# Performance work log

Measured on AMD Instinct MI355X. Metric: run time of the kernel, lower is better.

## Reference

```python
import jax, jax.numpy as jnp
from jax import lax
import numpy as np

NA, NC = 3, 1
CONF_THRESH, IOU_THRESH = 0.5, 0.5


def _conv(x, w, b, pad):
    y = lax.conv_general_dilated(x, w, (1, 1), [(pad, pad), (pad, pad)],
                                 dimension_numbers=('NCHW', 'OIHW', 'NCHW'))
    return y + b[None, :, None, None]


def _maxpool2(x):
    return lax.reduce_window(x, -jnp.inf, lax.max, (1, 1, 2, 2), (1, 1, 2, 2), 'VALID')


def _stream(x, w1, b1, w2, b2):
    x = _maxpool2(jax.nn.relu(_conv(x, w1, b1, 1)))
    x = _maxpool2(jax.nn.relu(_conv(x, w2, b2, 1)))
    return x


def _pairwise_iou(b):
    # b: [N,4] in (x1,y1,x2,y2); matches torchvision box_iou (no area clamp)
    x1, y1, x2, y2 = b[:, 0], b[:, 1], b[:, 2], b[:, 3]
    area = (x2 - x1) * (y2 - y1)
    ix1 = jnp.maximum(x1[:, None], x1[None, :])
    iy1 = jnp.maximum(y1[:, None], y1[None, :])
    ix2 = jnp.minimum(x2[:, None], x2[None, :])
    iy2 = jnp.minimum(y2[:, None], y2[None, :])
    inter = jnp.clip(ix2 - ix1, 0.0) * jnp.clip(iy2 - iy1, 0.0)
    return inter / (area[:, None] + area[None, :] - inter)


def _nms_keep(boxes, scores, conf_keep, iou_thresh):
    # Greedy NMS over a fixed, small N; returns bool keep mask (conf + NMS).
    n = boxes.shape[0]
    order = jnp.argsort(-jnp.where(conf_keep, scores, -jnp.inf))
    iou = _pairwise_iou(boxes[order])  # [N,N] in score order
    idx = jnp.arange(n)

    def body(i, state):
        keep, suppressed = state
        valid = jnp.logical_not(suppressed[i])
        keep = keep.at[i].set(valid)
        suppressed = suppressed | (valid & (iou[i] > iou_thresh) & (idx > i))
        return keep, suppressed

    keep_sorted, _ = lax.fori_loop(0, n, body,
                                   (jnp.zeros(n, bool), jnp.zeros(n, bool)))
    keep = jnp.zeros(n, bool).at[order].set(keep_sorted)
    return keep & conf_keep


def setup_inputs() -> dict:
    key = jax.random.key(0)
    ks = jax.random.split(key, 14)
    s = 0.05
    inp = {
        'x': jax.random.normal(ks[0], (8, 3, 512, 512), jnp.float32),
        'rgb_w1': jax.random.normal(ks[1], (32, 3, 3, 3), jnp.float32) * s,
        'rgb_b1': jnp.zeros((32,), jnp.float32),
        'rgb_w2': jax.random.normal(ks[2], (64, 32, 3, 3), jnp.float32) * s,
        'rgb_b2': jnp.zeros((64,), jnp.float32),
        'ir_w1': jax.random.normal(ks[3], (32, 3, 3, 3), jnp.float32) * s,
        'ir_b1': jnp.zeros((32,), jnp.float32),
        'ir_w2': jax.random.normal(ks[4], (64, 32, 3, 3), jnp.float32) * s,
        'ir_b2': jnp.zeros((64,), jnp.float32),
        'fuse_w': jax.random.normal(ks[5], (128, 128, 3, 3), jnp.float32) * s,
        'fuse_b': jnp.zeros((128,), jnp.float32),
        'det_w': jax.random.normal(ks[6], (NA * (5 + NC), 128, 1, 1), jnp.float32),
        'det_b': jax.random.normal(ks[7], (NA * (5 + NC),), jnp.float32),
    }
    return inp


def reference(x, rgb_w1, rgb_b1, rgb_w2, rgb_b2,
              ir_w1, ir_b1, ir_w2, ir_b2,
              fuse_w, fuse_b, det_w, det_b):
    f1 = _stream(x, rgb_w1, rgb_b1, rgb_w2, rgb_b2)   # [B,64,H/4,W/4]
    f2 = _stream(x, ir_w1, ir_b1, ir_w2, ir_b2)       # [B,64,H/4,W/4]
    f = jnp.concatenate([f1, f2], axis=1)             # [B,128,H/4,W/4]
    f = jax.nn.relu(_conv(f, fuse_w, fuse_b, 1))
    f = jnp.mean(f, axis=(2, 3), keepdims=True)       # AdaptiveAvgPool2d((1,1))
    p = _conv(f, det_w, det_b, 0)                     # [B,18,1,1]
    B, C, H, W = p.shape
    p = p.reshape(B, NA, 5 + NC, H, W).transpose(0, 1, 3, 4, 2)  # [B,na,H,W,5+nc]
    boxes = p[..., :4].reshape(B, -1, 4)              # [B, na*H*W, 4]
    scores = jax.nn.sigmoid(p[..., 4]).reshape(B, -1) # [B, na*H*W]
    conf_keep = scores > CONF_THRESH
    keep = jax.vmap(_nms_keep, in_axes=(0, 0, 0, None))(boxes, scores, conf_keep,
                                                        IOU_THRESH)
    # Fixed-shape equivalent of the per-image variable-length preds list:
    # preds[b] == boxes[b][keep[b]].
    return p, boxes, scores, keep
```

## Files before the change

kernel.cpp:

```cpp
#include <hip/hip_runtime.h>
#include <math.h>


typedef __bf16 bf16x8 __attribute__((ext_vector_type(8)));
typedef float f32x4 __attribute__((ext_vector_type(4)));

static __device__ __forceinline__ ushort f2bf(float f) {
    unsigned u = __float_as_uint(f);
    unsigned r = (u + 0x7fffu + ((u >> 16) & 1u)) >> 16;
    return (ushort)r;
}
static __device__ __forceinline__ float bf2f(ushort h) {
    return __uint_as_float(((unsigned)h) << 16);
}

__global__ __launch_bounds__(256) void conv1_pool(
    const float* __restrict__ x, const float* __restrict__ w,
    const float* __restrict__ bias, ushort* __restrict__ C1h,
    ushort* __restrict__ C1l)
{
    __shared__ float s[3 * 34 * 34];
    const int b = blockIdx.z;
    const int tileX = blockIdx.x, tileY = blockIdx.y;
    const int tid = threadIdx.x;
    const int tx = tid & 15, ty = tid >> 4;
    const int ih0 = tileY * 32 - 1, iw0 = tileX * 32 - 1;

    for (int i = tid; i < 3 * 34 * 34; i += 256) {
        int c = i / 1156, r = i % 1156;
        int y = r / 34, xx = r % 34;
        int ih = ih0 + y, iw = iw0 + xx;
        float v = 0.f;
        if (ih >= 0 && ih < 512 && iw >= 0 && iw < 512)
            v = x[((b * 3 + c) * 512 + ih) * 512 + iw];
        s[i] = v;
    }
    __syncthreads();

    float in[3][4][4];
#pragma unroll
    for (int c = 0; c < 3; ++c)
#pragma unroll
        for (int dy = 0; dy < 4; ++dy)
#pragma unroll
            for (int dx = 0; dx < 4; ++dx)
                in[c][dy][dx] = s[c * 1156 + (2 * ty + dy) * 34 + (2 * tx + dx)];

    const int oh = tileY * 16 + ty, ow = tileX * 16 + tx;
    __attribute__((aligned(16))) ushort hb[32];
    __attribute__((aligned(16))) ushort lb[32];
#pragma unroll
    for (int oc = 0; oc < 32; ++oc) {
        const float bv = bias[oc];
        float m = -INFINITY;
#pragma unroll
        for (int py = 0; py < 2; ++py)
#pragma unroll
            for (int px = 0; px < 2; ++px) {
                float a = 0.f;
#pragma unroll
                for (int c = 0; c < 3; ++c)
#pragma unroll
                    for (int ky = 0; ky < 3; ++ky)
#pragma unroll
                        for (int kx = 0; kx < 3; ++kx)
                            a = fmaf(w[((oc * 3 + c) * 3 + ky) * 3 + kx],
                                     in[c][py + ky][px + kx], a);
                m = fmaxf(m, a);
            }
        m = fmaxf(m + bv, 0.f);
        ushort h = f2bf(m);
        hb[oc] = h;
        lb[oc] = f2bf(m - bf2f(h));
    }
    size_t base = ((size_t)((b * 256 + oh) * 256 + ow)) << 5;
    uint4* dh = (uint4*)(C1h + base);
    uint4* dl = (uint4*)(C1l + base);
#pragma unroll
    for (int k = 0; k < 4; ++k) {
        dh[k] = *(const uint4*)&hb[k * 8];
        dl[k] = *(const uint4*)&lb[k * 8];
    }
}

__global__ __launch_bounds__(256) void conv2_mfma(
    const ushort* __restrict__ C1h, const ushort* __restrict__ C1l,
    const float* __restrict__ w2, const float* __restrict__ bias,
    ushort* __restrict__ Ahi, ushort* __restrict__ Alo, int stream_base)
{
    __shared__ char lds[73728];
    ushort* Bh = (ushort*)lds;
    ushort* Bl = (ushort*)(lds + 36864);
    float (*pool)[32][64] = (float (*)[32][64])lds;

    const int seg = blockIdx.x, Y = blockIdx.y, b = blockIdx.z;
    const int tid = threadIdx.x, wsub = tid >> 6, lane = tid & 63;
    const int n = lane & 15, q = lane >> 4;
    const int yc = 2 * Y + (wsub & 1);
    const int wx0 = seg * 128 + (wsub >> 1) * 64;

    const uint4 zero4 = make_uint4(0u, 0u, 0u, 0u);

    for (int i = tid; i < 18432; i += 256) {
        int t = i >> 11;
        int r = i & 2047;
        int oc = r >> 5, kk = r & 31;
        float v = w2[(oc * 32 + kk) * 9 + t];
        ushort h = f2bf(v);
        Bh[i] = h;
        Bl[i] = f2bf(v - bf2f(h));
    }

    auto loadA = [&](int t, uint4* aH, uint4* aL) {
        int ky = t / 3, kx = t - ky * 3;
        int yy = yc + ky - 1;
        bool yok = (yy >= 0) & (yy < 256);
#pragma unroll
        for (int mt = 0; mt < 4; ++mt) {
            int xp = wx0 + mt * 16 + n + kx - 1;
            bool ok = yok & (xp >= 0) & (xp < 256);
            int yyc = ok ? yy : 0, xpc = ok ? xp : 0;
            size_t off = (((size_t)((b * 256 + yyc) * 256 + xpc)) << 5) + q * 8;
            aH[mt] = ok ? *(const uint4*)(C1h + off) : zero4;
            aL[mt] = ok ? *(const uint4*)(C1l + off) : zero4;
        }
    };

    f32x4 acc[4][4];
#pragma unroll
    for (int mt = 0; mt < 4; ++mt)
#pragma unroll
        for (int nt = 0; nt < 4; ++nt) acc[mt][nt] = (f32x4){0.f, 0.f, 0.f, 0.f};

    uint4 aH[4], aL[4];
    loadA(0, aH, aL);
    __syncthreads();

    for (int t = 0; t < 9; ++t) {
        uint4 cH[4], cL[4];
#pragma unroll
        for (int mt = 0; mt < 4; ++mt) { cH[mt] = aH[mt]; cL[mt] = aL[mt]; }
        if (t + 1 < 9) loadA(t + 1, aH, aL);
        bf16x8 bh[4], bl[4];
#pragma unroll
        for (int nt = 0; nt < 4; ++nt) {
            int off = t * 2048 + (nt * 16 + n) * 32 + q * 8;
            bh[nt] = __builtin_bit_cast(bf16x8, *(const uint4*)&Bh[off]);
            bl[nt] = __builtin_bit_cast(bf16x8, *(const uint4*)&Bl[off]);
        }
#pragma unroll
        for (int mt = 0; mt < 4; ++mt) {
            bf16x8 ah = __builtin_bit_cast(bf16x8, cH[mt]);
#pragma unroll
            for (int nt = 0; nt < 4; ++nt)
                acc[mt][nt] = __builtin_amdgcn_mfma_f32_16x16x32_bf16(ah, bh[nt], acc[mt][nt], 0, 0, 0);
        }
#pragma unroll
        for (int mt = 0; mt < 4; ++mt) {
            bf16x8 ah = __builtin_bit_cast(bf16x8, cH[mt]);
#pragma unroll
            for (int nt = 0; nt < 4; ++nt)
                acc[mt][nt] = __builtin_amdgcn_mfma_f32_16x16x32_bf16(ah, bl[nt], acc[mt][nt], 0, 0, 0);
        }
#pragma unroll
        for (int mt = 0; mt < 4; ++mt) {
            bf16x8 al = __builtin_bit_cast(bf16x8, cL[mt]);
#pragma unroll
            for (int nt = 0; nt < 4; ++nt)
                acc[mt][nt] = __builtin_amdgcn_mfma_f32_16x16x32_bf16(al, bh[nt], acc[mt][nt], 0, 0, 0);
        }
    }

    __syncthreads();

#pragma unroll
    for (int mt = 0; mt < 4; ++mt)
#pragma unroll
        for (int nt = 0; nt < 4; ++nt) {
            int oc = nt * 16 + n;
            int plx = mt * 8 + q * 2;
            pool[wsub][plx][oc]     = fmaxf(acc[mt][nt][0], acc[mt][nt][1]);
            pool[wsub][plx + 1][oc] = fmaxf(acc[mt][nt][2], acc[mt][nt][3]);
        }
    __syncthreads();

    {
        int plx = tid >> 2, ocq = tid & 3;
        int wp = plx >> 5, pl = plx & 31;
        __attribute__((aligned(16))) ushort hb[16], lb[16];
#pragma unroll
        for (int e = 0; e < 16; ++e) {
            int oc = ocq * 16 + e;
            float v = fmaxf(pool[wp * 2][pl][oc], pool[wp * 2 + 1][pl][oc]);
            v = fmaxf(v + bias[oc], 0.f);
            ushort h = f2bf(v);
            hb[e] = h;
            lb[e] = f2bf(v - bf2f(h));
        }
        int gx = seg * 64 + plx;
        int cpl = (stream_base >> 5) + (ocq >> 1);
        int cho = (ocq & 1) * 16;
        size_t base = (((size_t)(((b * 4 + cpl) * 128 + Y) * 128 + gx)) << 5) + cho;
        uint4* dh = (uint4*)(Ahi + base);
        uint4* dl = (uint4*)(Alo + base);
        dh[0] = *(const uint4*)&hb[0];
        dh[1] = *(const uint4*)&hb[8];
        dl[0] = *(const uint4*)&lb[0];
        dl[1] = *(const uint4*)&lb[8];
    }
}

__global__ __launch_bounds__(256) void wprep(
    const float* __restrict__ fw, ushort* __restrict__ Whi,
    ushort* __restrict__ Wlo)
{
    int idx = blockIdx.x * 256 + threadIdx.x;
    if (idx >= 147456) return;
    int kk = idx & 31;
    int oc = (idx >> 5) & 127;
    int ct = idx >> 12;
    int c = ct / 9, t = ct - c * 9;
    int ic = c * 32 + kk;
    int ky = t / 3, kx = t - ky * 3;
    float v = fw[((oc * 128 + ic) * 3 + ky) * 3 + kx];
    ushort h = f2bf(v);
    Whi[idx] = h;
    Wlo[idx] = f2bf(v - bf2f(h));
}

__global__ __launch_bounds__(256, 2) void fuse_mfma(
    const ushort* __restrict__ Ahi, const ushort* __restrict__ Alo,
    const ushort* __restrict__ Whi, const ushort* __restrict__ Wlo,
    const float* __restrict__ bias, float* __restrict__ featsum)
{
    __shared__ float partial[4][128];
    const int b = blockIdx.x, ypair = blockIdx.y;
    const int tid = threadIdx.x, wsub = tid >> 6, lane = tid & 63;
    const int n = lane & 15, q = lane >> 4;
    const int y = ypair * 2 + (wsub >> 1);
    const int xbase = (wsub & 1) * 64;

    f32x4 acc[4][8];
#pragma unroll
    for (int mt = 0; mt < 4; ++mt)
#pragma unroll
        for (int g = 0; g < 8; ++g) acc[mt][g] = (f32x4){0.f, 0.f, 0.f, 0.f};

    const uint4 zero4 = make_uint4(0u, 0u, 0u, 0u);

    auto loadA = [&](int tc, uint4* oh, uint4* ol) {
        int c = tc / 9, t = tc - c * 9;
        int ky = t / 3, kx = t - ky * 3;
        int yy = y + ky - 1;
        bool yok = (yy >= 0) & (yy < 128);
#pragma unroll
        for (int mt = 0; mt < 4; ++mt) {
            int xp = xbase + mt * 16 + n + kx - 1;
            bool ok = yok & (xp >= 0) & (xp < 128);
            int yyc = ok ? yy : 0, xpc = ok ? xp : 0;
            size_t aoff = (((size_t)(((b * 4 + c) * 128 + yyc) * 128 + xpc)) << 5) + q * 8;
            oh[mt] = ok ? *(const uint4*)(Ahi + aoff) : zero4;
            ol[mt] = ok ? *(const uint4*)(Alo + aoff) : zero4;
        }
    };

    uint4 pAh[4], pAl[4];
    loadA(0, pAh, pAl);

    const int boff = n * 32 + q * 8;

    for (int tc = 0; tc < 36; ++tc) {
        uint4 cAh[4], cAl[4];
#pragma unroll
        for (int mt = 0; mt < 4; ++mt) { cAh[mt] = pAh[mt]; cAl[mt] = pAl[mt]; }
        if (tc + 1 < 36) loadA(tc + 1, pAh, pAl);
        const ushort* bhp = Whi + tc * 4096 + boff;
        const ushort* blp = Wlo + tc * 4096 + boff;
#pragma unroll
        for (int g = 0; g < 8; ++g) {
            bf16x8 bh = __builtin_bit_cast(bf16x8, *(const uint4*)(bhp + g * 512));
            bf16x8 bl = __builtin_bit_cast(bf16x8, *(const uint4*)(blp + g * 512));
#pragma unroll
            for (int mt = 0; mt < 4; ++mt) {
                bf16x8 ah = __builtin_bit_cast(bf16x8, cAh[mt]);
                acc[mt][g] = __builtin_amdgcn_mfma_f32_16x16x32_bf16(ah, bh, acc[mt][g], 0, 0, 0);
            }
#pragma unroll
            for (int mt = 0; mt < 4; ++mt) {
                bf16x8 ah = __builtin_bit_cast(bf16x8, cAh[mt]);
                acc[mt][g] = __builtin_amdgcn_mfma_f32_16x16x32_bf16(ah, bl, acc[mt][g], 0, 0, 0);
            }
#pragma unroll
            for (int mt = 0; mt < 4; ++mt) {
                bf16x8 al = __builtin_bit_cast(bf16x8, cAl[mt]);
                acc[mt][g] = __builtin_amdgcn_mfma_f32_16x16x32_bf16(al, bh, acc[mt][g], 0, 0, 0);
            }
        }
    }

#pragma unroll
    for (int g = 0; g < 8; ++g) {
        float bv = bias[g * 16 + n];
        float v = 0.f;
#pragma unroll
        for (int mt = 0; mt < 4; ++mt)
#pragma unroll
            for (int r = 0; r < 4; ++r) v += fmaxf(acc[mt][g][r] + bv, 0.f);
        v += __shfl_xor(v, 16);
        v += __shfl_xor(v, 32);
        if (lane < 16) partial[wsub][g * 16 + lane] = v;
    }
    __syncthreads();
    if (tid < 128) {
        float v = partial[0][tid] + partial[1][tid] + partial[2][tid] + partial[3][tid];
        atomicAdd(&featsum[b * 128 + tid], v);
    }
}

__global__ void det_nms(const float* __restrict__ featsum,
                        const float* __restrict__ dw, const float* __restrict__ db,
                        float* __restrict__ out)
{
    const int b = threadIdx.x;
    if (b >= 8) return;
    const float inv = 1.0f / 16384.0f;

    float p[18];
    for (int j = 0; j < 18; ++j) {
        float a = db[j];
        const float* wp = &dw[j * 128];
        const float* f = &featsum[b * 128];
        for (int c = 0; c < 128; ++c) a = fmaf(wp[c], f[c] * inv, a);
        p[j] = a;
    }
    for (int a = 0; a < 3; ++a)
        for (int e = 0; e < 6; ++e) out[b * 18 + a * 6 + e] = p[a * 6 + e];

    float bx[3][4], sc[3];
    bool ck[3];
    for (int a = 0; a < 3; ++a) {
        for (int k = 0; k < 4; ++k) {
            bx[a][k] = p[a * 6 + k];
            out[144 + b * 12 + a * 4 + k] = bx[a][k];
        }
        float sg = 1.f / (1.f + expf(-p[a * 6 + 4]));
        sc[a] = sg;
        ck[a] = sg > 0.5f;
        out[240 + b * 3 + a] = sg;
    }

    float key[3];
    int order[3];
    bool used[3] = {false, false, false};
    for (int a = 0; a < 3; ++a) key[a] = ck[a] ? sc[a] : -INFINITY;
    for (int i = 0; i < 3; ++i) {
        int best = -1;
        float bk = 0.f;
        for (int a = 0; a < 3; ++a) {
            if (used[a]) continue;
            if (best < 0 || key[a] > bk) { best = a; bk = key[a]; }
        }
        order[i] = best;
        used[best] = true;
    }

    float X1[3], Y1[3], X2[3], Y2[3], AR[3];
    for (int i = 0; i < 3; ++i) {
        int o = order[i];
        X1[i] = bx[o][0]; Y1[i] = bx[o][1];
        X2[i] = bx[o][2]; Y2[i] = bx[o][3];
        AR[i] = (X2[i] - X1[i]) * (Y2[i] - Y1[i]);
    }
    bool suppressed[3] = {false, false, false}, keep_s[3];
    for (int i = 0; i < 3; ++i) {
        bool valid = !suppressed[i];
        keep_s[i] = valid;
        if (valid) {
            for (int j = i + 1; j < 3; ++j) {
                float ix1 = fmaxf(X1[i], X1[j]), iy1 = fmaxf(Y1[i], Y1[j]);
                float ix2 = fminf(X2[i], X2[j]), iy2 = fminf(Y2[i], Y2[j]);
                float inter = fmaxf(ix2 - ix1, 0.f) * fmaxf(iy2 - iy1, 0.f);
                float iou = inter / (AR[i] + AR[j] - inter);
                if (iou > 0.5f) suppressed[j] = true;
            }
        }
    }
    bool keep[3];
    for (int i = 0; i < 3; ++i) keep[order[i]] = keep_s[i];
    for (int a = 0; a < 3; ++a)
        out[264 + b * 3 + a] = (keep[a] && ck[a]) ? 1.f : 0.f;
}

__global__ void zero_feat(float* __restrict__ p)
{
    int i = blockIdx.x * 256 + threadIdx.x;
    if (i < 1024) p[i] = 0.f;
}

extern "C" void kernel_launch(void* const* d_in, const int* in_sizes, int n_in,
                              void* d_out, int out_size, void* d_ws, size_t ws_size,
                              hipStream_t stream)
{
    const float* x      = (const float*)d_in[0];
    const float* rgb_w1 = (const float*)d_in[1];
    const float* rgb_b1 = (const float*)d_in[2];
    const float* rgb_w2 = (const float*)d_in[3];
    const float* rgb_b2 = (const float*)d_in[4];
    const float* ir_w1  = (const float*)d_in[5];
    const float* ir_b1  = (const float*)d_in[6];
    const float* ir_w2  = (const float*)d_in[7];
    const float* ir_b2  = (const float*)d_in[8];
    const float* fuse_w = (const float*)d_in[9];
    const float* fuse_b = (const float*)d_in[10];
    const float* det_w  = (const float*)d_in[11];
    const float* det_b  = (const float*)d_in[12];
    float* out = (float*)d_out;

    char* ws = (char*)d_ws;
    ushort* C1h  = (ushort*)(ws);
    ushort* C1l  = (ushort*)(ws + 33554432);
    ushort* Whi  = (ushort*)(ws);
    ushort* Wlo  = (ushort*)(ws + 294912);
    float*  feat = (float*)(ws + 589824);
    ushort* Ahi  = (ushort*)(ws + 67108864);
    ushort* Alo  = (ushort*)(ws + 100663296);

    dim3 blk(256);
    hipLaunchKernelGGL(conv1_pool, dim3(16, 16, 8), blk, 0, stream, x, rgb_w1, rgb_b1, C1h, C1l);
    hipLaunchKernelGGL(conv2_mfma, dim3(2, 128, 8), blk, 0, stream, C1h, C1l, rgb_w2, rgb_b2, Ahi, Alo, 0);
    hipLaunchKernelGGL(conv1_pool, dim3(16, 16, 8), blk, 0, stream, x, ir_w1, ir_b1, C1h, C1l);
    hipLaunchKernelGGL(conv2_mfma, dim3(2, 128, 8), blk, 0, stream, C1h, C1l, ir_w2, ir_b2, Ahi, Alo, 64);
    hipLaunchKernelGGL(wprep, dim3(576), blk, 0, stream, fuse_w, Whi, Wlo);
    hipLaunchKernelGGL(zero_feat, dim3(4), blk, 0, stream, feat);
    hipLaunchKernelGGL(fuse_mfma, dim3(8, 64), blk, 0, stream, Ahi, Alo, Whi, Wlo, fuse_b, feat);
    hipLaunchKernelGGL(det_nms, dim3(1), dim3(64), 0, stream, feat, det_w, det_b, out);
}
```

Measured before the change: 569.0 us.

## Halve conv2 LDS via two-phase weight staging; split fuse conv output channels

conv2_mfma now stages its bf16 hi/lo weight tiles in two phases (taps 0-4, then taps 5-8), shrinking LDS from 72KB to 40KB so more blocks can be resident per CU, at the cost of two extra barriers mid-loop. fuse_mfma splits the 128 output channels across a new grid z-dimension of 2, halving the accumulator registers per thread and raising launch bounds to 3 blocks per SM. The split doubles the A-tile reads from global memory across blocks and doubles the number of atomics.

```diff
diff --git a/kernel.cpp b/kernel.cpp
--- a/kernel.cpp
+++ b/kernel.cpp
@@ -88,9 +88,9 @@
     const float* __restrict__ w2, const float* __restrict__ bias,
     ushort* __restrict__ Ahi, ushort* __restrict__ Alo, int stream_base)
 {
-    __shared__ char lds[73728];
+    __shared__ char lds[40960];
     ushort* Bh = (ushort*)lds;
-    ushort* Bl = (ushort*)(lds + 36864);
+    ushort* Bl = (ushort*)(lds + 20480);
     float (*pool)[32][64] = (float (*)[32][64])lds;
 
     const int seg = blockIdx.x, Y = blockIdx.y, b = blockIdx.z;
@@ -101,15 +101,15 @@
 
     const uint4 zero4 = make_uint4(0u, 0u, 0u, 0u);
 
-    for (int i = tid; i < 18432; i += 256) {
-        int t = i >> 11;
-        int r = i & 2047;
-        int oc = r >> 5, kk = r & 31;
-        float v = w2[(oc * 32 + kk) * 9 + t];
-        ushort h = f2bf(v);
-        Bh[i] = h;
-        Bl[i] = f2bf(v - bf2f(h));
-    }
+    auto stageB = [&](int t0, int ntap) {
+        for (int i = tid; i < ntap * 2048; i += 256) {
+            int t = t0 + (i >> 11), r = i & 2047;
+            float v = w2[r * 9 + t];
+            ushort h = f2bf(v);
+            Bh[i] = h;
+            Bl[i] = f2bf(v - bf2f(h));
+        }
+    };
 
     auto loadA = [&](int t, uint4* aH, uint4* aL) {
         int ky = t / 3, kx = t - ky * 3;
@@ -134,9 +134,16 @@
 
     uint4 aH[4], aL[4];
     loadA(0, aH, aL);
+    stageB(0, 5);
     __syncthreads();
 
     for (int t = 0; t < 9; ++t) {
+        if (t == 5) {
+            __syncthreads();
+            stageB(5, 4);
+            __syncthreads();
+        }
+        const int rel = (t < 5) ? t : t - 5;
         uint4 cH[4], cL[4];
 #pragma unroll
         for (int mt = 0; mt < 4; ++mt) { cH[mt] = aH[mt]; cL[mt] = aL[mt]; }
@@ -144,7 +151,7 @@
         bf16x8 bh[4], bl[4];
 #pragma unroll
         for (int nt = 0; nt < 4; ++nt) {
-            int off = t * 2048 + (nt * 16 + n) * 32 + q * 8;
+            int off = rel * 2048 + (nt * 16 + n) * 32 + q * 8;
             bh[nt] = __builtin_bit_cast(bf16x8, *(const uint4*)&Bh[off]);
             bl[nt] = __builtin_bit_cast(bf16x8, *(const uint4*)&Bl[off]);
         }
@@ -228,27 +235,27 @@
     Wlo[idx] = f2bf(v - bf2f(h));
 }
 
-__global__ __launch_bounds__(256, 2) void fuse_mfma(
+__global__ __launch_bounds__(256, 3) void fuse_mfma(
     const ushort* __restrict__ Ahi, const ushort* __restrict__ Alo,
     const ushort* __restrict__ Whi, const ushort* __restrict__ Wlo,
     const float* __restrict__ bias, float* __restrict__ featsum)
 {
-    __shared__ float partial[4][128];
-    const int b = blockIdx.x, ypair = blockIdx.y;
+    __shared__ float partial[4][64];
+    const int b = blockIdx.x, ypair = blockIdx.y, oh = blockIdx.z;
     const int tid = threadIdx.x, wsub = tid >> 6, lane = tid & 63;
     const int n = lane & 15, q = lane >> 4;
     const int y = ypair * 2 + (wsub >> 1);
     const int xbase = (wsub & 1) * 64;
 
-    f32x4 acc[4][8];
+    f32x4 acc[4][4];
 #pragma unroll
     for (int mt = 0; mt < 4; ++mt)
 #pragma unroll
-        for (int g = 0; g < 8; ++g) acc[mt][g] = (f32x4){0.f, 0.f, 0.f, 0.f};
+        for (int g = 0; g < 4; ++g) acc[mt][g] = (f32x4){0.f, 0.f, 0.f, 0.f};
 
     const uint4 zero4 = make_uint4(0u, 0u, 0u, 0u);
 
-    auto loadA = [&](int tc, uint4* oh, uint4* ol) {
+    auto loadA = [&](int tc, uint4* ohh, uint4* oll) {
         int c = tc / 9, t = tc - c * 9;
         int ky = t / 3, kx = t - ky * 3;
         int yy = y + ky - 1;
@@ -259,15 +266,15 @@
             bool ok = yok & (xp >= 0) & (xp < 128);
             int yyc = ok ? yy : 0, xpc = ok ? xp : 0;
             size_t aoff = (((size_t)(((b * 4 + c) * 128 + yyc) * 128 + xpc)) << 5) + q * 8;
-            oh[mt] = ok ? *(const uint4*)(Ahi + aoff) : zero4;
-            ol[mt] = ok ? *(const uint4*)(Alo + aoff) : zero4;
+            ohh[mt] = ok ? *(const uint4*)(Ahi + aoff) : zero4;
+            oll[mt] = ok ? *(const uint4*)(Alo + aoff) : zero4;
         }
     };
 
     uint4 pAh[4], pAl[4];
     loadA(0, pAh, pAl);
 
-    const int boff = n * 32 + q * 8;
+    const int boff = (oh * 64 + n) * 32 + q * 8;
 
     for (int tc = 0; tc < 36; ++tc) {
         uint4 cAh[4], cAl[4];
@@ -277,7 +284,7 @@
         const ushort* bhp = Whi + tc * 4096 + boff;
         const ushort* blp = Wlo + tc * 4096 + boff;
 #pragma unroll
-        for (int g = 0; g < 8; ++g) {
+        for (int g = 0; g < 4; ++g) {
             bf16x8 bh = __builtin_bit_cast(bf16x8, *(const uint4*)(bhp + g * 512));
             bf16x8 bl = __builtin_bit_cast(bf16x8, *(const uint4*)(blp + g * 512));
 #pragma unroll
@@ -299,8 +306,8 @@
     }
 
 #pragma unroll
-    for (int g = 0; g < 8; ++g) {
-        float bv = bias[g * 16 + n];
+    for (int g = 0; g < 4; ++g) {
+        float bv = bias[oh * 64 + g * 16 + n];
         float v = 0.f;
 #pragma unroll
         for (int mt = 0; mt < 4; ++mt)
@@ -311,9 +318,9 @@
         if (lane < 16) partial[wsub][g * 16 + lane] = v;
     }
     __syncthreads();
-    if (tid < 128) {
+    if (tid < 64) {
         float v = partial[0][tid] + partial[1][tid] + partial[2][tid] + partial[3][tid];
-        atomicAdd(&featsum[b * 128 + tid], v);
+        atomicAdd(&featsum[b * 128 + oh * 64 + tid], v);
     }
 }
 
@@ -432,6 +439,6 @@
     hipLaunchKernelGGL(conv2_mfma, dim3(2, 128, 8), blk, 0, stream, C1h, C1l, ir_w2, ir_b2, Ahi, Alo, 64);
     hipLaunchKernelGGL(wprep, dim3(576), blk, 0, stream, fuse_w, Whi, Wlo);
     hipLaunchKernelGGL(zero_feat, dim3(4), blk, 0, stream, feat);
-    hipLaunchKernelGGL(fuse_mfma, dim3(8, 64), blk, 0, stream, Ahi, Alo, Whi, Wlo, fuse_b, feat);
+    hipLaunchKernelGGL(fuse_mfma, dim3(8, 64, 2), blk, 0, stream, Ahi, Alo, Whi, Wlo, fuse_b, feat);
     hipLaunchKernelGGL(det_nms, dim3(1), dim3(64), 0, stream, feat, det_w, det_b, out);
 }
```

Measured after the change: 610.6 us. 7.3% more time.

## Stage conv2 weights in two LDS phases and prefetch fuse weights in registers

Applied to the files above, without the earlier changes.

conv2_mfma now stages the split-bf16 weights into LDS in two chunks (taps 0-4, then 5-8). This cuts shared memory per block from 72KB to 40KB so more blocks can be resident per CU, at the cost of two extra barriers and a mid-loop weight reload. fuse_mfma now prefetches the global weight fragments four steps ahead through a rotating register buffer instead of loading them just before use. The prefetch reads past the last tap, so the workspace offsets for Wlo and feat were padded to keep those reads in bounds.

```diff
diff --git a/kernel.cpp b/kernel.cpp
--- a/kernel.cpp
+++ b/kernel.cpp
@@ -88,9 +88,9 @@
     const float* __restrict__ w2, const float* __restrict__ bias,
     ushort* __restrict__ Ahi, ushort* __restrict__ Alo, int stream_base)
 {
-    __shared__ char lds[73728];
+    __shared__ char lds[40960];
     ushort* Bh = (ushort*)lds;
-    ushort* Bl = (ushort*)(lds + 36864);
+    ushort* Bl = (ushort*)(lds + 20480);
     float (*pool)[32][64] = (float (*)[32][64])lds;
 
     const int seg = blockIdx.x, Y = blockIdx.y, b = blockIdx.z;
@@ -101,15 +101,15 @@
 
     const uint4 zero4 = make_uint4(0u, 0u, 0u, 0u);
 
-    for (int i = tid; i < 18432; i += 256) {
-        int t = i >> 11;
-        int r = i & 2047;
-        int oc = r >> 5, kk = r & 31;
-        float v = w2[(oc * 32 + kk) * 9 + t];
-        ushort h = f2bf(v);
-        Bh[i] = h;
-        Bl[i] = f2bf(v - bf2f(h));
-    }
+    auto stageB = [&](int t0, int ntap) {
+        for (int i = tid; i < ntap * 2048; i += 256) {
+            int t = t0 + (i >> 11), r = i & 2047;
+            float v = w2[r * 9 + t];
+            ushort h = f2bf(v);
+            Bh[i] = h;
+            Bl[i] = f2bf(v - bf2f(h));
+        }
+    };
 
     auto loadA = [&](int t, uint4* aH, uint4* aL) {
         int ky = t / 3, kx = t - ky * 3;
@@ -134,9 +134,16 @@
 
     uint4 aH[4], aL[4];
     loadA(0, aH, aL);
+    stageB(0, 5);
     __syncthreads();
 
     for (int t = 0; t < 9; ++t) {
+        if (t == 5) {
+            __syncthreads();
+            stageB(5, 4);
+            __syncthreads();
+        }
+        const int rel = (t < 5) ? t : t - 5;
         uint4 cH[4], cL[4];
 #pragma unroll
         for (int mt = 0; mt < 4; ++mt) { cH[mt] = aH[mt]; cL[mt] = aL[mt]; }
@@ -144,7 +151,7 @@
         bf16x8 bh[4], bl[4];
 #pragma unroll
         for (int nt = 0; nt < 4; ++nt) {
-            int off = t * 2048 + (nt * 16 + n) * 32 + q * 8;
+            int off = rel * 2048 + (nt * 16 + n) * 32 + q * 8;
             bh[nt] = __builtin_bit_cast(bf16x8, *(const uint4*)&Bh[off]);
             bl[nt] = __builtin_bit_cast(bf16x8, *(const uint4*)&Bl[off]);
         }
@@ -267,19 +274,31 @@
     uint4 pAh[4], pAl[4];
     loadA(0, pAh, pAl);
 
-    const int boff = n * 32 + q * 8;
+    const ushort* WhiB = Whi + n * 32 + q * 8;
+    const ushort* WloB = Wlo + n * 32 + q * 8;
+
+    uint4 nBh[4], nBl[4];
+#pragma unroll
+    for (int j = 0; j < 4; ++j) {
+        nBh[j] = *(const uint4*)(WhiB + j * 512);
+        nBl[j] = *(const uint4*)(WloB + j * 512);
+    }
 
     for (int tc = 0; tc < 36; ++tc) {
         uint4 cAh[4], cAl[4];
 #pragma unroll
         for (int mt = 0; mt < 4; ++mt) { cAh[mt] = pAh[mt]; cAl[mt] = pAl[mt]; }
         if (tc + 1 < 36) loadA(tc + 1, pAh, pAl);
-        const ushort* bhp = Whi + tc * 4096 + boff;
-        const ushort* blp = Wlo + tc * 4096 + boff;
 #pragma unroll
         for (int g = 0; g < 8; ++g) {
-            bf16x8 bh = __builtin_bit_cast(bf16x8, *(const uint4*)(bhp + g * 512));
-            bf16x8 bl = __builtin_bit_cast(bf16x8, *(const uint4*)(blp + g * 512));
+            const int slot = g & 3;
+            bf16x8 bh = __builtin_bit_cast(bf16x8, nBh[slot]);
+            bf16x8 bl = __builtin_bit_cast(bf16x8, nBl[slot]);
+            {
+                size_t off = (size_t)(tc * 8 + g + 4) * 512;
+                nBh[slot] = *(const uint4*)(WhiB + off);
+                nBl[slot] = *(const uint4*)(WloB + off);
+            }
 #pragma unroll
             for (int mt = 0; mt < 4; ++mt) {
                 bf16x8 ah = __builtin_bit_cast(bf16x8, cAh[mt]);
@@ -420,8 +439,8 @@
     ushort* C1h  = (ushort*)(ws);
     ushort* C1l  = (ushort*)(ws + 33554432);
     ushort* Whi  = (ushort*)(ws);
-    ushort* Wlo  = (ushort*)(ws + 294912);
-    float*  feat = (float*)(ws + 589824);
+    ushort* Wlo  = (ushort*)(ws + 299008);
+    float*  feat = (float*)(ws + 598016);
     ushort* Ahi  = (ushort*)(ws + 67108864);
     ushort* Alo  = (ushort*)(ws + 100663296);
 
```

Result: faster. 544.6 us (-4.3%).
